# Optimization experiments

Measured on AMD Instinct MI355X. Metric: run time of the kernel, lower is better.

## Reference

```python
import jax, jax.numpy as jnp
import numpy as np

MUL = 16          # multiplicity of every irrep block
N = 131072        # number of nodes

# orthonormal traceless-symmetric 3x3 basis, divided by sqrt(5).
_s = 1.0 / np.sqrt(2.0)
_M = np.zeros((5, 3, 3), dtype=np.float32)
_M[0, 0, 1] = _M[0, 1, 0] = _s
_M[1, 0, 2] = _M[1, 2, 0] = _s
_M[2, 1, 2] = _M[2, 2, 1] = _s
_M[3, 0, 0] = _s; _M[3, 1, 1] = -_s
_M[4] = np.diag([-1.0, -1.0, 2.0]).astype(np.float32) / np.sqrt(6.0)
C112 = jnp.asarray(np.transpose(_M, (1, 2, 0)) / np.sqrt(5.0))  # (3,3,5)

# e3nn TensorProduct normalization: irrep_normalization='component'
# (alpha = 2l_out+1), path_normalization='element' (divide by sum of
# mul_u*mul_v over paths into the same output irrep). 0e output receives
# two paths -> 2*MUL^2; 1o and 2e each receive one path -> MUL^2.
A000 = float(np.sqrt(1.0 / (2.0 * MUL * MUL)))                    # 0e x 0e -> 0e (w3j = 1)
A110 = float(np.sqrt(1.0 / (2.0 * MUL * MUL)) / np.sqrt(3.0))     # 1o x 1o -> 0e (w3j = d_ij/sqrt(3))
A101 = float(np.sqrt(3.0 / (MUL * MUL)) / np.sqrt(3.0))           # 1o x 0e -> 1o (w3j = d_ik/sqrt(3))
A112 = float(np.sqrt(5.0 / (MUL * MUL)))                          # 1o x 1o -> 2e


def setup_inputs() -> dict:
    key = jax.random.key(0)
    ks = jax.random.split(key, 6)
    f = lambda k, s: jax.random.normal(k, s, dtype=jnp.float32)
    return {
        "node_feats": f(ks[0], (N, 4 * MUL)),
        "node_messages": f(ks[1], (N, 4 * MUL)),
        "w000": f(ks[2], (MUL, MUL, MUL)),
        "w101": f(ks[3], (MUL, MUL, MUL)),
        "w110": f(ks[4], (MUL, MUL, MUL)),
        "w112": f(ks[5], (MUL, MUL, MUL)),
    }


def _tensor_square(x, w000, w101, w110, w112):
    """e3nn o3.TensorSquare('16x0e+16x1o', '16x0e+16x1o+16x2e') with 'uvw' weighted paths."""
    n = x.shape[0]
    x0 = x[:, :MUL]                          # (n, u)     l=0 block
    x1 = x[:, MUL:].reshape(n, MUL, 3)       # (n, u, i)  l=1 block (mul-major)

    # --- 0e output ---
    out0 = A000 * jnp.einsum('uvw,nu,nv->nw', w000, x0, x0)
    out0 = out0 + A110 * jnp.einsum('uvw,nui,nvi->nw', w110, x1, x1)

    # --- 1o output ---
    out1 = A101 * jnp.einsum('uvw,nuk,nv->nwk', w101, x1, x0)

    # --- 2e output (staged to keep intermediates small) ---
    t1 = jnp.einsum('nvj,ijk->nvik', x1, C112)        # (n, v, i, 5)
    t = jnp.einsum('nui,nvik->nuvk', x1, t1)          # (n, u, v, 5)
    out2 = A112 * jnp.einsum('uvw,nuvk->nwk', w112, t)

    return jnp.concatenate(
        [out0, out1.reshape(n, 3 * MUL), out2.reshape(n, 5 * MUL)], axis=1
    )  # (n, 144)


def reference(node_feats, node_messages, w000, w101, w110, w112):
    # SimpleNodeBlock: sum all nodewise tensors, then tensor square.
    return _tensor_square(node_feats + node_messages, w000, w101, w110, w112)
```

## Files before the change

kernel.cpp:

```cpp
#include <hip/hip_runtime.h>

#define MUL 16
#define NTILE 30
#define NCHUNK 6

typedef __bf16 bf16x8 __attribute__((ext_vector_type(8)));
typedef float  f32x2  __attribute__((ext_vector_type(2)));
typedef float  f32x4  __attribute__((ext_vector_type(4)));

__device__ __forceinline__ void group_uvs(int g, int& u, int& vs) {
    if (g < 16) { u = g >> 1; vs = u + ((g & 1) << 3); }
    else        { u = g - 8;  vs = u; }
}

__global__ void prep_weights(const float* __restrict__ w000,
                             const float* __restrict__ w101,
                             const float* __restrict__ w110,
                             const float* __restrict__ w112,
                             __bf16* __restrict__ wt) {
    const int gid = blockIdx.x * 256 + threadIdx.x;
    if (gid >= NTILE * 64) return;
    const int T = gid >> 6, lane = gid & 63;
    const int q = lane >> 4, w = lane & 15;

    const float A000   = 0.044194173824159216f;
    const float A110   = 0.025515518153991442f;
    const float A101   = 0.0625f;
    const float A112C1 = 0.044194173824159216f;

    bf16x8 frag = {};
    if (T < 12) {
        const int c = T >> 1, h = T & 1;
        int u, vs; group_uvs(4 * c + q, u, vs);
#pragma unroll
        for (int i = 0; i < 4; ++i) {
            const int v = vs + 4 * h + i;
            if (v < 16) {
                const int uvw = (u * MUL + v) * MUL + w;
                const int vuw = (v * MUL + u) * MUL + w;
                float f000, f110;
                if (u == v) { f000 = A000 * w000[uvw]; f110 = A110 * w110[uvw]; }
                else        { f000 = A000 * (w000[uvw] + w000[vuw]);
                              f110 = A110 * (w110[uvw] + w110[vuw]); }
                frag[2 * i]     = (__bf16)f000;
                frag[2 * i + 1] = (__bf16)f110;
            }
        }
    } else if (T < 24) {
        const int c = (T - 12) >> 1, h = (T - 12) & 1;
        int u, vs; group_uvs(4 * c + q, u, vs);
#pragma unroll
        for (int i = 0; i < 4; ++i) {
            const int v = vs + 4 * h + i;
            if (v < 16) {
                const int uvw = (u * MUL + v) * MUL + w;
                const int vuw = (v * MUL + u) * MUL + w;
                frag[2 * i]     = (__bf16)(A101 * w101[uvw]);
                frag[2 * i + 1] = (__bf16)((u == v) ? 0.f : A101 * w101[vuw]);
            }
        }
    } else {
        const int c = T - 24;
        int u, vs; group_uvs(4 * c + q, u, vs);
#pragma unroll
        for (int e = 0; e < 8; ++e) {
            const int v = vs + e;
            if (v < 16) {
                const int uvw = (u * MUL + v) * MUL + w;
                const int vuw = (v * MUL + u) * MUL + w;
                const float f112 = (u == v) ? A112C1 * w112[uvw]
                                            : A112C1 * (w112[uvw] + w112[vuw]);
                frag[e] = (__bf16)f112;
            }
        }
    }
    ((bf16x8*)wt)[T * 64 + lane] = frag;
}

#define SQ3f  1.7320508075688772f
#define ISQ3f 0.5773502691896258f

template<int J>
__device__ __forceinline__ void do_pair(int vs, const float* __restrict__ xrow,
        const float4 xu,
        bf16x8& fS, bf16x8& f0, bf16x8& f1, bf16x8& f2,
        bf16x8& t0, bf16x8& t1, bf16x8& t2, bf16x8& t3, bf16x8& t4) {
    int v = vs + J;
    v = v < 15 ? v : 15;
    const float4 xv = *(const float4*)(xrow + 4 * v);

    const f32x2 U01 = {xu.x, xu.y};
    const f32x2 U23 = {xu.z, xu.w};
    const f32x2 U10 = {xu.y, xu.x};
    const f32x2 V01 = {xv.x, xv.y};
    const f32x2 V23 = {xv.z, xv.w};
    const f32x2 V10 = {xv.y, xv.x};
    const f32x2 V32 = {xv.w, xv.z};

    const f32x2 P1 = U01 * V01;
    const f32x2 P2 = U23 * V23;
    const f32x2 P3 = U01 * V23;
    const f32x2 P4 = U23 * V01;
    const f32x2 P5 = U01 * V32;
    const f32x2 P6 = U23 * V10;
    const f32x2 P7 = U23 * V32;
    const f32x2 P8 = U10 * V01;

    const float o00 = P1[1], o11 = P2[0], o22 = P2[1];
    const float s1 = (o00 + o11) + o22;

    constexpr int s2 = (J & 3) * 2;
    fS[s2]     = (__bf16)P1[0];  fS[s2 + 1] = (__bf16)s1;
    f0[s2]     = (__bf16)P8[0];  f0[s2 + 1] = (__bf16)P8[1];
    f1[s2]     = (__bf16)P4[0];  f1[s2 + 1] = (__bf16)P3[0];
    f2[s2]     = (__bf16)P6[1];  f2[s2 + 1] = (__bf16)P5[0];
    t0[J] = (__bf16)(P5[1] + P6[0]);
    t1[J] = (__bf16)(P3[1] + P4[1]);
    t2[J] = (__bf16)(P7[0] + P7[1]);
    t3[J] = (__bf16)(o00 - o11);
    t4[J] = (__bf16)(SQ3f * o22 - ISQ3f * s1);
}

__launch_bounds__(64, 4)
__global__ void tsq_kernel(const float* __restrict__ feats,
                           const float* __restrict__ msgs,
                           const __bf16* __restrict__ wtiles,
                           float* __restrict__ out) {
    __shared__ __align__(16) float xq[16 * 68];
    __shared__ __align__(16) float ep[16 * 144];

    const int tid = threadIdx.x;
    const long long blockNode = (long long)blockIdx.x * 16;

    {
        const float4* f4p = (const float4*)(feats + blockNode * 64);
        const float4* m4p = (const float4*)(msgs  + blockNode * 64);
#pragma unroll
        for (int r = 0; r < 4; ++r) {
            const int li = r * 64 + tid;
            const int nd = li >> 4, f4 = li & 15;
            const float4 a = f4p[li];
            const float4 b = m4p[li];
            const float vals[4] = {a.x + b.x, a.y + b.y, a.z + b.z, a.w + b.w};
#pragma unroll
            for (int jj = 0; jj < 4; ++jj) {
                const int f = 4 * f4 + jj;
                int dst;
                if (f < 16) dst = nd * 68 + 4 * f;
                else {
                    const int g = f - 16;
                    const int v3 = (g * 171) >> 9;
                    dst = nd * 68 + 4 * v3 + 1 + (g - 3 * v3);
                }
                xq[dst] = vals[jj];
            }
        }
    }
    __syncthreads();

    const int lane = tid;
    const int m = lane & 15, q = lane >> 4;
    const float* xrow = xq + m * 68;
    const bf16x8* wb = (const bf16x8*)wtiles;

    f32x4 accS  = {0.f, 0.f, 0.f, 0.f};
    f32x4 accP0 = {0.f, 0.f, 0.f, 0.f};
    f32x4 accP1 = {0.f, 0.f, 0.f, 0.f};
    f32x4 accP2 = {0.f, 0.f, 0.f, 0.f};
    f32x4 accT0 = {0.f, 0.f, 0.f, 0.f};
    f32x4 accT1 = {0.f, 0.f, 0.f, 0.f};
    f32x4 accT2 = {0.f, 0.f, 0.f, 0.f};
    f32x4 accT3 = {0.f, 0.f, 0.f, 0.f};
    f32x4 accT4 = {0.f, 0.f, 0.f, 0.f};

    bf16x8 bS0 = wb[0 * 64 + lane];
    bf16x8 bS1 = wb[1 * 64 + lane];
    bf16x8 bP0 = wb[12 * 64 + lane];
    bf16x8 bP1 = wb[13 * 64 + lane];
    bf16x8 bT  = wb[24 * 64 + lane];

#pragma unroll
    for (int c = 0; c < NCHUNK; ++c) {
        bf16x8 nS0 = {}, nS1 = {}, nP0 = {}, nP1 = {}, nT = {};
        if (c + 1 < NCHUNK) {
            nS0 = wb[(2 * c + 2) * 64 + lane];
            nS1 = wb[(2 * c + 3) * 64 + lane];
            nP0 = wb[(14 + 2 * c) * 64 + lane];
            nP1 = wb[(15 + 2 * c) * 64 + lane];
            nT  = wb[(25 + c) * 64 + lane];
        }

        int u, vs;
        if (c < 4) { u = 2 * c + (q >> 1); vs = u + ((q & 1) << 3); }
        else       { u = 4 * c - 8 + q;    vs = u; }
        const float4 xu = *(const float4*)(xrow + 4 * u);

        bf16x8 t0 = {}, t1 = {}, t2 = {}, t3 = {}, t4 = {};
        {
            bf16x8 fS, f0, f1, f2;
            do_pair<0>(vs, xrow, xu, fS, f0, f1, f2, t0, t1, t2, t3, t4);
            do_pair<1>(vs, xrow, xu, fS, f0, f1, f2, t0, t1, t2, t3, t4);
            do_pair<2>(vs, xrow, xu, fS, f0, f1, f2, t0, t1, t2, t3, t4);
            do_pair<3>(vs, xrow, xu, fS, f0, f1, f2, t0, t1, t2, t3, t4);
            accS  = __builtin_amdgcn_mfma_f32_16x16x32_bf16(fS, bS0, accS,  0, 0, 0);
            accP0 = __builtin_amdgcn_mfma_f32_16x16x32_bf16(f0, bP0, accP0, 0, 0, 0);
            accP1 = __builtin_amdgcn_mfma_f32_16x16x32_bf16(f1, bP0, accP1, 0, 0, 0);
            accP2 = __builtin_amdgcn_mfma_f32_16x16x32_bf16(f2, bP0, accP2, 0, 0, 0);
        }
        {
            bf16x8 fS, f0, f1, f2;
            do_pair<4>(vs, xrow, xu, fS, f0, f1, f2, t0, t1, t2, t3, t4);
            do_pair<5>(vs, xrow, xu, fS, f0, f1, f2, t0, t1, t2, t3, t4);
            do_pair<6>(vs, xrow, xu, fS, f0, f1, f2, t0, t1, t2, t3, t4);
            do_pair<7>(vs, xrow, xu, fS, f0, f1, f2, t0, t1, t2, t3, t4);
            accS  = __builtin_amdgcn_mfma_f32_16x16x32_bf16(fS, bS1, accS,  0, 0, 0);
            accP0 = __builtin_amdgcn_mfma_f32_16x16x32_bf16(f0, bP1, accP0, 0, 0, 0);
            accP1 = __builtin_amdgcn_mfma_f32_16x16x32_bf16(f1, bP1, accP1, 0, 0, 0);
            accP2 = __builtin_amdgcn_mfma_f32_16x16x32_bf16(f2, bP1, accP2, 0, 0, 0);
        }
        accT0 = __builtin_amdgcn_mfma_f32_16x16x32_bf16(t0, bT, accT0, 0, 0, 0);
        accT1 = __builtin_amdgcn_mfma_f32_16x16x32_bf16(t1, bT, accT1, 0, 0, 0);
        accT2 = __builtin_amdgcn_mfma_f32_16x16x32_bf16(t2, bT, accT2, 0, 0, 0);
        accT3 = __builtin_amdgcn_mfma_f32_16x16x32_bf16(t3, bT, accT3, 0, 0, 0);
        accT4 = __builtin_amdgcn_mfma_f32_16x16x32_bf16(t4, bT, accT4, 0, 0, 0);

        bS0 = nS0; bS1 = nS1; bP0 = nP0; bP1 = nP1; bT = nT;
    }

#pragma unroll
    for (int r = 0; r < 4; ++r) {
        float* eb = ep + (q * 4 + r) * 144;
        eb[m]              = accS[r];
        eb[16 + 3 * m + 0] = accP0[r];
        eb[16 + 3 * m + 1] = accP1[r];
        eb[16 + 3 * m + 2] = accP2[r];
        eb[64 + 5 * m + 0] = accT0[r];
        eb[64 + 5 * m + 1] = accT1[r];
        eb[64 + 5 * m + 2] = accT2[r];
        eb[64 + 5 * m + 3] = accT3[r];
        eb[64 + 5 * m + 4] = accT4[r];
    }
    __syncthreads();

    {
        const float4* ep4 = (const float4*)ep;
        float4* ob4 = (float4*)(out + blockNode * 144);
#pragma unroll
        for (int l = 0; l < 9; ++l)
            ob4[l * 64 + lane] = ep4[l * 64 + lane];
    }
}

extern "C" void kernel_launch(void* const* d_in, const int* in_sizes, int n_in,
                              void* d_out, int out_size, void* d_ws, size_t ws_size,
                              hipStream_t stream) {
    const float* feats = (const float*)d_in[0];
    const float* msgs  = (const float*)d_in[1];
    const float* w000  = (const float*)d_in[2];
    const float* w101  = (const float*)d_in[3];
    const float* w110  = (const float*)d_in[4];
    const float* w112  = (const float*)d_in[5];
    __bf16* wt = (__bf16*)d_ws;
    float* out = (float*)d_out;

    const int n = in_sizes[0] / (4 * MUL);

    prep_weights<<<(NTILE * 64 + 255) / 256, 256, 0, stream>>>(w000, w101, w110, w112, wt);
    tsq_kernel<<<n / 16, 64, 0, stream>>>(feats, msgs, wt, out);
}
```

Baseline: 153.9 us.

## Use 4-wave persistent blocks with grid-stride tiles and per-wave shared scratch

The kernel moves from one 64-thread block per 16 nodes to persistent 256-thread blocks of four waves, each wave handling 16 nodes of a 64-node tile in a grid-stride loop capped at 1024 blocks. The input staging now has each lane gather scalar feature and message values directly into the interleaved float4 layout, replacing the earlier float4-coalesced loads. One shared buffer per wave is reused for both the input and the epilogue staging. This is meant to cut block launch overhead and let weight loads be reused across tiles. In exchange it adds block-wide barriers on each tile and uses uncoalesced strided global loads.

```diff
diff --git a/kernel.cpp b/kernel.cpp
--- a/kernel.cpp
+++ b/kernel.cpp
@@ -121,133 +121,132 @@
     t4[J] = (__bf16)(SQ3f * o22 - ISQ3f * s1);
 }
 
-__launch_bounds__(64, 4)
+__launch_bounds__(256, 4)
 __global__ void tsq_kernel(const float* __restrict__ feats,
                            const float* __restrict__ msgs,
                            const __bf16* __restrict__ wtiles,
-                           float* __restrict__ out) {
-    __shared__ __align__(16) float xq[16 * 68];
-    __shared__ __align__(16) float ep[16 * 144];
-
-    const int tid = threadIdx.x;
-    const long long blockNode = (long long)blockIdx.x * 16;
-
-    {
-        const float4* f4p = (const float4*)(feats + blockNode * 64);
-        const float4* m4p = (const float4*)(msgs  + blockNode * 64);
+                           float* __restrict__ out,
+                           int ntiles) {
+    __shared__ __align__(16) float smem[4][2304];
+
+    const int tid  = threadIdx.x;
+    const int lane = tid & 63;
+    const int wid  = tid >> 6;
+    float* sw = smem[wid];
+
+    const int m = lane & 15, q = lane >> 4;
+    const float* xrow = sw + m * 68;
+    const bf16x8* wb = (const bf16x8*)wtiles;
+
+    for (int tile = blockIdx.x; tile < ntiles; tile += gridDim.x) {
+        const long long waveNode = (long long)tile * 64 + wid * 16;
+
+        {
+            const int v = lane & 15, g = lane >> 4;
+#pragma unroll
+            for (int k = 0; k < 4; ++k) {
+                const int nd = g * 4 + k;
+                const float* fp = feats + (waveNode + nd) * 64;
+                const float* mp = msgs  + (waveNode + nd) * 64;
+                float4 qd;
+                qd.x = fp[v]          + mp[v];
+                qd.y = fp[16 + 3 * v] + mp[16 + 3 * v];
+                qd.z = fp[17 + 3 * v] + mp[17 + 3 * v];
+                qd.w = fp[18 + 3 * v] + mp[18 + 3 * v];
+                *(float4*)&sw[nd * 68 + 4 * v] = qd;
+            }
+        }
+        __syncthreads();
+
+        f32x4 accS  = {0.f, 0.f, 0.f, 0.f};
+        f32x4 accP0 = {0.f, 0.f, 0.f, 0.f};
+        f32x4 accP1 = {0.f, 0.f, 0.f, 0.f};
+        f32x4 accP2 = {0.f, 0.f, 0.f, 0.f};
+        f32x4 accT0 = {0.f, 0.f, 0.f, 0.f};
+        f32x4 accT1 = {0.f, 0.f, 0.f, 0.f};
+        f32x4 accT2 = {0.f, 0.f, 0.f, 0.f};
+        f32x4 accT3 = {0.f, 0.f, 0.f, 0.f};
+        f32x4 accT4 = {0.f, 0.f, 0.f, 0.f};
+
+        bf16x8 bS0 = wb[0 * 64 + lane];
+        bf16x8 bS1 = wb[1 * 64 + lane];
+        bf16x8 bP0 = wb[12 * 64 + lane];
+        bf16x8 bP1 = wb[13 * 64 + lane];
+        bf16x8 bT  = wb[24 * 64 + lane];
+
+#pragma unroll
+        for (int c = 0; c < NCHUNK; ++c) {
+            bf16x8 nS0 = {}, nS1 = {}, nP0 = {}, nP1 = {}, nT = {};
+            if (c + 1 < NCHUNK) {
+                nS0 = wb[(2 * c + 2) * 64 + lane];
+                nS1 = wb[(2 * c + 3) * 64 + lane];
+                nP0 = wb[(14 + 2 * c) * 64 + lane];
+                nP1 = wb[(15 + 2 * c) * 64 + lane];
+                nT  = wb[(25 + c) * 64 + lane];
+            }
+
+            int u, vs;
+            if (c < 4) { u = 2 * c + (q >> 1); vs = u + ((q & 1) << 3); }
+            else       { u = 4 * c - 8 + q;    vs = u; }
+            const float4 xu = *(const float4*)(xrow + 4 * u);
+
+            bf16x8 t0 = {}, t1 = {}, t2 = {}, t3 = {}, t4 = {};
+            {
+                bf16x8 fS, f0, f1, f2;
+                do_pair<0>(vs, xrow, xu, fS, f0, f1, f2, t0, t1, t2, t3, t4);
+                do_pair<1>(vs, xrow, xu, fS, f0, f1, f2, t0, t1, t2, t3, t4);
+                do_pair<2>(vs, xrow, xu, fS, f0, f1, f2, t0, t1, t2, t3, t4);
+                do_pair<3>(vs, xrow, xu, fS, f0, f1, f2, t0, t1, t2, t3, t4);
+                accS  = __builtin_amdgcn_mfma_f32_16x16x32_bf16(fS, bS0, accS,  0, 0, 0);
+                accP0 = __builtin_amdgcn_mfma_f32_16x16x32_bf16(f0, bP0, accP0, 0, 0, 0);
+                accP1 = __builtin_amdgcn_mfma_f32_16x16x32_bf16(f1, bP0, accP1, 0, 0, 0);
+                accP2 = __builtin_amdgcn_mfma_f32_16x16x32_bf16(f2, bP0, accP2, 0, 0, 0);
+            }
+            {
+                bf16x8 fS, f0, f1, f2;
+                do_pair<4>(vs, xrow, xu, fS, f0, f1, f2, t0, t1, t2, t3, t4);
+                do_pair<5>(vs, xrow, xu, fS, f0, f1, f2, t0, t1, t2, t3, t4);
+                do_pair<6>(vs, xrow, xu, fS, f0, f1, f2, t0, t1, t2, t3, t4);
+                do_pair<7>(vs, xrow, xu, fS, f0, f1, f2, t0, t1, t2, t3, t4);
+                accS  = __builtin_amdgcn_mfma_f32_16x16x32_bf16(fS, bS1, accS,  0, 0, 0);
+                accP0 = __builtin_amdgcn_mfma_f32_16x16x32_bf16(f0, bP1, accP0, 0, 0, 0);
+                accP1 = __builtin_amdgcn_mfma_f32_16x16x32_bf16(f1, bP1, accP1, 0, 0, 0);
+                accP2 = __builtin_amdgcn_mfma_f32_16x16x32_bf16(f2, bP1, accP2, 0, 0, 0);
+            }
+            accT0 = __builtin_amdgcn_mfma_f32_16x16x32_bf16(t0, bT, accT0, 0, 0, 0);
+            accT1 = __builtin_amdgcn_mfma_f32_16x16x32_bf16(t1, bT, accT1, 0, 0, 0);
+            accT2 = __builtin_amdgcn_mfma_f32_16x16x32_bf16(t2, bT, accT2, 0, 0, 0);
+            accT3 = __builtin_amdgcn_mfma_f32_16x16x32_bf16(t3, bT, accT3, 0, 0, 0);
+            accT4 = __builtin_amdgcn_mfma_f32_16x16x32_bf16(t4, bT, accT4, 0, 0, 0);
+
+            bS0 = nS0; bS1 = nS1; bP0 = nP0; bP1 = nP1; bT = nT;
+        }
+
+        __syncthreads();
+
 #pragma unroll
         for (int r = 0; r < 4; ++r) {
-            const int li = r * 64 + tid;
-            const int nd = li >> 4, f4 = li & 15;
-            const float4 a = f4p[li];
-            const float4 b = m4p[li];
-            const float vals[4] = {a.x + b.x, a.y + b.y, a.z + b.z, a.w + b.w};
-#pragma unroll
-            for (int jj = 0; jj < 4; ++jj) {
-                const int f = 4 * f4 + jj;
-                int dst;
-                if (f < 16) dst = nd * 68 + 4 * f;
-                else {
-                    const int g = f - 16;
-                    const int v3 = (g * 171) >> 9;
-                    dst = nd * 68 + 4 * v3 + 1 + (g - 3 * v3);
-                }
-                xq[dst] = vals[jj];
-            }
-        }
-    }
-    __syncthreads();
-
-    const int lane = tid;
-    const int m = lane & 15, q = lane >> 4;
-    const float* xrow = xq + m * 68;
-    const bf16x8* wb = (const bf16x8*)wtiles;
-
-    f32x4 accS  = {0.f, 0.f, 0.f, 0.f};
-    f32x4 accP0 = {0.f, 0.f, 0.f, 0.f};
-    f32x4 accP1 = {0.f, 0.f, 0.f, 0.f};
-    f32x4 accP2 = {0.f, 0.f, 0.f, 0.f};
-    f32x4 accT0 = {0.f, 0.f, 0.f, 0.f};
-    f32x4 accT1 = {0.f, 0.f, 0.f, 0.f};
-    f32x4 accT2 = {0.f, 0.f, 0.f, 0.f};
-    f32x4 accT3 = {0.f, 0.f, 0.f, 0.f};
-    f32x4 accT4 = {0.f, 0.f, 0.f, 0.f};
-
-    bf16x8 bS0 = wb[0 * 64 + lane];
-    bf16x8 bS1 = wb[1 * 64 + lane];
-    bf16x8 bP0 = wb[12 * 64 + lane];
-    bf16x8 bP1 = wb[13 * 64 + lane];
-    bf16x8 bT  = wb[24 * 64 + lane];
-
-#pragma unroll
-    for (int c = 0; c < NCHUNK; ++c) {
-        bf16x8 nS0 = {}, nS1 = {}, nP0 = {}, nP1 = {}, nT = {};
-        if (c + 1 < NCHUNK) {
-            nS0 = wb[(2 * c + 2) * 64 + lane];
-            nS1 = wb[(2 * c + 3) * 64 + lane];
-            nP0 = wb[(14 + 2 * c) * 64 + lane];
-            nP1 = wb[(15 + 2 * c) * 64 + lane];
-            nT  = wb[(25 + c) * 64 + lane];
-        }
-
-        int u, vs;
-        if (c < 4) { u = 2 * c + (q >> 1); vs = u + ((q & 1) << 3); }
-        else       { u = 4 * c - 8 + q;    vs = u; }
-        const float4 xu = *(const float4*)(xrow + 4 * u);
-
-        bf16x8 t0 = {}, t1 = {}, t2 = {}, t3 = {}, t4 = {};
+            float* eb = sw + (q * 4 + r) * 144;
+            eb[m]              = accS[r];
+            eb[16 + 3 * m + 0] = accP0[r];
+            eb[16 + 3 * m + 1] = accP1[r];
+            eb[16 + 3 * m + 2] = accP2[r];
+            eb[64 + 5 * m + 0] = accT0[r];
+            eb[64 + 5 * m + 1] = accT1[r];
+            eb[64 + 5 * m + 2] = accT2[r];
+            eb[64 + 5 * m + 3] = accT3[r];
+            eb[64 + 5 * m + 4] = accT4[r];
+        }
+        __syncthreads();
+
         {
-            bf16x8 fS, f0, f1, f2;
-            do_pair<0>(vs, xrow, xu, fS, f0, f1, f2, t0, t1, t2, t3, t4);
-            do_pair<1>(vs, xrow, xu, fS, f0, f1, f2, t0, t1, t2, t3, t4);
-            do_pair<2>(vs, xrow, xu, fS, f0, f1, f2, t0, t1, t2, t3, t4);
-            do_pair<3>(vs, xrow, xu, fS, f0, f1, f2, t0, t1, t2, t3, t4);
-            accS  = __builtin_amdgcn_mfma_f32_16x16x32_bf16(fS, bS0, accS,  0, 0, 0);
-            accP0 = __builtin_amdgcn_mfma_f32_16x16x32_bf16(f0, bP0, accP0, 0, 0, 0);
-            accP1 = __builtin_amdgcn_mfma_f32_16x16x32_bf16(f1, bP0, accP1, 0, 0, 0);
-            accP2 = __builtin_amdgcn_mfma_f32_16x16x32_bf16(f2, bP0, accP2, 0, 0, 0);
-        }
-        {
-            bf16x8 fS, f0, f1, f2;
-            do_pair<4>(vs, xrow, xu, fS, f0, f1, f2, t0, t1, t2, t3, t4);
-            do_pair<5>(vs, xrow, xu, fS, f0, f1, f2, t0, t1, t2, t3, t4);
-            do_pair<6>(vs, xrow, xu, fS, f0, f1, f2, t0, t1, t2, t3, t4);
-            do_pair<7>(vs, xrow, xu, fS, f0, f1, f2, t0, t1, t2, t3, t4);
-            accS  = __builtin_amdgcn_mfma_f32_16x16x32_bf16(fS, bS1, accS,  0, 0, 0);
-            accP0 = __builtin_amdgcn_mfma_f32_16x16x32_bf16(f0, bP1, accP0, 0, 0, 0);
-            accP1 = __builtin_amdgcn_mfma_f32_16x16x32_bf16(f1, bP1, accP1, 0, 0, 0);
-            accP2 = __builtin_amdgcn_mfma_f32_16x16x32_bf16(f2, bP1, accP2, 0, 0, 0);
-        }
-        accT0 = __builtin_amdgcn_mfma_f32_16x16x32_bf16(t0, bT, accT0, 0, 0, 0);
-        accT1 = __builtin_amdgcn_mfma_f32_16x16x32_bf16(t1, bT, accT1, 0, 0, 0);
-        accT2 = __builtin_amdgcn_mfma_f32_16x16x32_bf16(t2, bT, accT2, 0, 0, 0);
-        accT3 = __builtin_amdgcn_mfma_f32_16x16x32_bf16(t3, bT, accT3, 0, 0, 0);
-        accT4 = __builtin_amdgcn_mfma_f32_16x16x32_bf16(t4, bT, accT4, 0, 0, 0);
-
-        bS0 = nS0; bS1 = nS1; bP0 = nP0; bP1 = nP1; bT = nT;
-    }
-
-#pragma unroll
-    for (int r = 0; r < 4; ++r) {
-        float* eb = ep + (q * 4 + r) * 144;
-        eb[m]              = accS[r];
-        eb[16 + 3 * m + 0] = accP0[r];
-        eb[16 + 3 * m + 1] = accP1[r];
-        eb[16 + 3 * m + 2] = accP2[r];
-        eb[64 + 5 * m + 0] = accT0[r];
-        eb[64 + 5 * m + 1] = accT1[r];
-        eb[64 + 5 * m + 2] = accT2[r];
-        eb[64 + 5 * m + 3] = accT3[r];
-        eb[64 + 5 * m + 4] = accT4[r];
-    }
-    __syncthreads();
-
-    {
-        const float4* ep4 = (const float4*)ep;
-        float4* ob4 = (float4*)(out + blockNode * 144);
-#pragma unroll
-        for (int l = 0; l < 9; ++l)
-            ob4[l * 64 + lane] = ep4[l * 64 + lane];
+            const float4* ep4 = (const float4*)sw;
+            float4* ob4 = (float4*)(out + waveNode * 144);
+#pragma unroll
+            for (int l = 0; l < 9; ++l)
+                ob4[l * 64 + lane] = ep4[l * 64 + lane];
+        }
+        __syncthreads();
     }
 }
 
@@ -264,7 +263,9 @@
     float* out = (float*)d_out;
 
     const int n = in_sizes[0] / (4 * MUL);
+    const int ntiles = n / 64;
+    const int grid = ntiles < 1024 ? ntiles : 1024;
 
     prep_weights<<<(NTILE * 64 + 255) / 256, 256, 0, stream>>>(w000, w101, w110, w112, wt);
-    tsq_kernel<<<n / 16, 64, 0, stream>>>(feats, msgs, wt, out);
-}
+    tsq_kernel<<<grid, 256, 0, stream>>>(feats, msgs, wt, out, ntiles);
+}
```

New measurement: 295.1 us. 1.92x slower.
